# Kernel tuning notes

Hardware: AMD Instinct MI355X
Metric: run time of the kernel (lower is better)

Reference implementation:

```python
import jax, jax.numpy as jnp
import numpy as np

SPATIAL_SCALE = 0.25
N, C, H, W = 8, 256, 128, 128
P = 100000
IMG = 512.0  # image-space extent (H / spatial_scale)


def setup_inputs() -> dict:
    key = jax.random.key(0)
    k1, k2, k3, k4 = jax.random.split(key, 4)
    features = jax.random.normal(k1, (N, C, H, W), dtype=jnp.float32)
    batch_idx = jax.random.randint(k2, (P,), 0, N).astype(jnp.float32)
    xy = jax.random.uniform(k3, (P, 2), dtype=jnp.float32) * IMG
    rois = jnp.concatenate([batch_idx[:, None], xy], axis=1)  # [P,3]: (b, x, y)
    return {"features": features, "rois": rois}


def _interp(features, rois, spatial_scale):
    n, c, h, w = features.shape
    b = rois[:, 0].astype(jnp.int32)
    x = rois[:, 1] * spatial_scale
    y = rois[:, 2] * spatial_scale
    # RoIAlign-style bilinear interpolation with boundary handling
    valid = (y >= -1.0) & (y <= h) & (x >= -1.0) & (x <= w)
    y = jnp.maximum(y, 0.0)
    x = jnp.maximum(x, 0.0)
    y_low = jnp.floor(y).astype(jnp.int32)
    x_low = jnp.floor(x).astype(jnp.int32)
    y_at_edge = y_low >= h - 1
    x_at_edge = x_low >= w - 1
    y_low = jnp.minimum(y_low, h - 1)
    x_low = jnp.minimum(x_low, w - 1)
    y_high = jnp.where(y_at_edge, y_low, y_low + 1)
    x_high = jnp.where(x_at_edge, x_low, x_low + 1)
    y = jnp.where(y_at_edge, y_low.astype(y.dtype), y)
    x = jnp.where(x_at_edge, x_low.astype(x.dtype), x)
    ly = y - y_low
    lx = x - x_low
    hy = 1.0 - ly
    hx = 1.0 - lx
    w1 = (hy * hx)[:, None]  # [P,1]
    w2 = (hy * lx)[:, None]
    w3 = (ly * hx)[:, None]
    w4 = (ly * lx)[:, None]
    # fancy-index gather: [P, C] per corner
    v1 = features[b, :, y_low, x_low]
    v2 = features[b, :, y_low, x_high]
    v3 = features[b, :, y_high, x_low]
    v4 = features[b, :, y_high, x_high]
    out = w1 * v1 + w2 * v2 + w3 * v3 + w4 * v4  # [P, C]
    return jnp.where(valid[:, None], out, 0.0)


def reference(features, rois):
    return _interp(features, rois, SPATIAL_SCALE)
```

## Files before the change

kernel.cpp:

```cpp
#include <hip/hip_runtime.h>

#define SCALE   0.25f
#define NBATCH  8
#define CCH     256
#define HH      128
#define WW      128
#define NBUCK   (NBATCH * HH)
#define CAP     160

#define CG      64
#define NCG     (CCH / CG)


__global__ __launch_bounds__(1024) void k_bin(
    const float* __restrict__ rois, int* __restrict__ cnt,
    int4* __restrict__ slots, int P)
{
    __shared__ int lhist[NBUCK];
    __shared__ int lbase[NBUCK];
    const int t = threadIdx.x;
    lhist[t] = 0;
    __syncthreads();

    int p = blockIdx.x * 1024 + t;
    int mybk = -1, mypos = 0;
    int4 myrec = make_int4(0, 0, 0, 0);
    if (p < P) {
        float fb = rois[3 * p];
        float fx = rois[3 * p + 1] * SCALE;
        float fy = rois[3 * p + 2] * SCALE;
        int b = (int)fb;
        bool valid = (fy >= -1.0f) && (fy <= (float)HH) &&
                     (fx >= -1.0f) && (fx <= (float)WW);
        float y = fmaxf(fy, 0.0f);
        float x = fmaxf(fx, 0.0f);
        int ylo = (int)floorf(y);
        int xlo = (int)floorf(x);
        float yf = y, xf = x;
        int xhi;
        if (ylo >= HH - 1) { ylo = HH - 1; yf = (float)ylo; }
        if (xlo >= WW - 1) { xlo = WW - 1; xhi = WW - 1; xf = (float)xlo; }
        else               { xhi = xlo + 1; }
        float ly = yf - (float)ylo;
        float lx = xf - (float)xlo;
        unsigned pk = (unsigned)xlo | ((unsigned)xhi << 8) | (valid ? 0u : 0x80000000u);
        int bk = b * HH + ylo;
        mybk  = bk;
        mypos = atomicAdd(&lhist[bk], 1);
        myrec = make_int4(p, (int)pk, __float_as_int(lx), __float_as_int(ly));
    }
    __syncthreads();
    int h = lhist[t];
    lbase[t] = h ? atomicAdd(&cnt[t], h) : 0;
    __syncthreads();
    if (mybk >= 0) {
        int idx = lbase[mybk] + mypos;
        if (idx < CAP) slots[mybk * CAP + idx] = myrec;
    }
}

__global__ __launch_bounds__(1024, 8) void k_main(
    const float* __restrict__ feat, const int4* __restrict__ slots,
    const int* __restrict__ cnt_arr, float* __restrict__ out)
{
    const int bk = blockIdx.x & (NBUCK - 1);
    const int cg = blockIdx.x >> 10;
    const int cnt = min(cnt_arr[bk], CAP);
    if (cnt == 0) return;
    const int b  = bk >> 7;
    const int yl = bk & 127;
    const int yh = min(yl + 1, HH - 1);

    __shared__ __align__(16) float lds[2 * 128 * 64];
    float4* lds4 = (float4*)lds;

    const int t = threadIdx.x;

    {
        const int xq  = t & 31;
        const int cq  = (t >> 5) & 15;
        const int row = t >> 9;
        const int y   = row ? yh : yl;
        const float* g = feat + ((size_t)(b * CCH + cg * CG + 4 * cq) * HH + y) * WW + 4 * xq;
        float4 f0 = *(const float4*)(g);
        float4 f1 = *(const float4*)(g + HH * WW);
        float4 f2 = *(const float4*)(g + 2 * HH * WW);
        float4 f3 = *(const float4*)(g + 3 * HH * WW);
        const int slot = (cq + xq) & 15;
        float4* d = &lds4[(size_t)row * 2048 + (4 * xq) * 16 + slot];
        d[0]  = make_float4(f0.x, f1.x, f2.x, f3.x);
        d[16] = make_float4(f0.y, f1.y, f2.y, f3.y);
        d[32] = make_float4(f0.z, f1.z, f2.z, f3.z);
        d[48] = make_float4(f0.w, f1.w, f2.w, f3.w);
    }

    const int wv   = t >> 6;
    const int lane = t & 63;
    const int sub  = lane >> 4;
    const int cq   = lane & 15;
    const int4* sb = slots + bk * CAP;

    int  ii = wv * 4;
    int4 rc = make_int4(0, 0, 0, 0);
    if (ii < cnt) rc = sb[min(ii + sub, cnt - 1)];
    __syncthreads();

    for (; ii < cnt; ii += 64) {
        int4 r = rc;
        int jn = ii + 64;
        if (jn < cnt) rc = sb[min(jn + sub, cnt - 1)];

        bool act = (ii + sub < cnt);
        unsigned pk = (unsigned)r.y;
        float lx = __int_as_float(r.z);
        float ly = __int_as_float(r.w);
        float s  = ((int)pk < 0) ? 0.0f : 1.0f;
        float hy  = (1.0f - ly) * s;
        float lys = ly * s;
        float hx  = 1.0f - lx;
        float w1 = hy * hx, w2 = hy * lx, w3 = lys * hx, w4 = lys * lx;
        int xlo = pk & 255;
        int xhi = (pk >> 8) & 255;
        int alo = xlo * 16 + ((cq + (xlo >> 2)) & 15);
        int ahi = xhi * 16 + ((cq + (xhi >> 2)) & 15);

        float4 v1 = lds4[alo],        v2 = lds4[ahi];
        float4 v3 = lds4[2048 + alo], v4 = lds4[2048 + ahi];
        float4 o;
        o.x = w1 * v1.x + w2 * v2.x + w3 * v3.x + w4 * v4.x;
        o.y = w1 * v1.y + w2 * v2.y + w3 * v3.y + w4 * v4.y;
        o.z = w1 * v1.z + w2 * v2.z + w3 * v3.z + w4 * v4.z;
        o.w = w1 * v1.w + w2 * v2.w + w3 * v3.w + w4 * v4.w;

        if (act)
            *(float4*)(out + (size_t)r.x * CCH + cg * CG + 4 * cq) = o;
    }
}

extern "C" void kernel_launch(void* const* d_in, const int* in_sizes, int n_in,
                              void* d_out, int out_size, void* d_ws, size_t ws_size,
                              hipStream_t stream) {
    const float* feat = (const float*)d_in[0];
    const float* rois = (const float*)d_in[1];
    float* out = (float*)d_out;
    const int P = in_sizes[1] / 3;

    int*  cnt   = (int*)d_ws;
    int4* slots = (int4*)((char*)d_ws + NBUCK * sizeof(int));

    hipMemsetAsync(cnt, 0, NBUCK * sizeof(int), stream);
    const int bb = (P + 1023) / 1024;
    k_bin<<<bb, 1024, 0, stream>>>(rois, cnt, slots, P);
    k_main<<<NCG * NBUCK, 1024, 0, stream>>>(feat, slots, cnt, out);
}
```

Measured before the change: 235.1 us.

## Process 16 consecutive row buckets per block with a ring-buffered feature-row pipeline

Each block now handles a run of 16 y-buckets for one batch and channel group instead of a single bucket. It keeps a 4-slot shared-memory ring of feature rows, so adjacent buckets reuse the shared row and global loads of upcoming rows overlap with interpolation of the current one. This removes the duplicate load of each row (previously loaded as both y_high and y_low) and cuts block launch overhead. The cost is fewer blocks (256 versus 4096), which lowers parallelism and risks load imbalance, plus a barrier per row.

```diff
diff --git a/kernel.cpp b/kernel.cpp
--- a/kernel.cpp
+++ b/kernel.cpp
@@ -5,11 +5,14 @@
 #define CCH     256
 #define HH      128
 #define WW      128
+#define HW      (HH * WW)
 #define NBUCK   (NBATCH * HH)
 #define CAP     160
 
 #define CG      64
 #define NCG     (CCH / CG)
+#define BPB     16
+#define NSLOT   4
 
 
 __global__ __launch_bounds__(1024) void k_bin(
@@ -59,58 +62,54 @@
     }
 }
 
-__global__ __launch_bounds__(1024, 8) void k_main(
+struct R4 { float4 a, b, c, d; };
+
+__global__ __launch_bounds__(1024, 4) void k_main(
     const float* __restrict__ feat, const int4* __restrict__ slots,
     const int* __restrict__ cnt_arr, float* __restrict__ out)
 {
-    const int bk = blockIdx.x & (NBUCK - 1);
-    const int cg = blockIdx.x >> 10;
-    const int cnt = min(cnt_arr[bk], CAP);
-    if (cnt == 0) return;
-    const int b  = bk >> 7;
-    const int yl = bk & 127;
-    const int yh = min(yl + 1, HH - 1);
-
-    __shared__ __align__(16) float lds[2 * 128 * 64];
-    float4* lds4 = (float4*)lds;
-
-    const int t = threadIdx.x;
-
-    {
-        const int xq  = t & 31;
-        const int cq  = (t >> 5) & 15;
-        const int row = t >> 9;
-        const int y   = row ? yh : yl;
-        const float* g = feat + ((size_t)(b * CCH + cg * CG + 4 * cq) * HH + y) * WW + 4 * xq;
-        float4 f0 = *(const float4*)(g);
-        float4 f1 = *(const float4*)(g + HH * WW);
-        float4 f2 = *(const float4*)(g + 2 * HH * WW);
-        float4 f3 = *(const float4*)(g + 3 * HH * WW);
-        const int slot = (cq + xq) & 15;
-        float4* d = &lds4[(size_t)row * 2048 + (4 * xq) * 16 + slot];
-        d[0]  = make_float4(f0.x, f1.x, f2.x, f3.x);
-        d[16] = make_float4(f0.y, f1.y, f2.y, f3.y);
-        d[32] = make_float4(f0.z, f1.z, f2.z, f3.z);
-        d[48] = make_float4(f0.w, f1.w, f2.w, f3.w);
-    }
-
+    const int grp = blockIdx.x & (NBATCH * (HH / BPB) - 1);
+    const int cg  = blockIdx.x >> 6;
+    const int b   = grp >> 3;
+    const int y0  = (grp & 7) * BPB;
+    const int bk0 = b * HH + y0;
+
+    __shared__ __align__(16) float4 ring[NSLOT][WW][16];
+    __shared__ int scnt[BPB];
+
+    const int t    = threadIdx.x;
     const int wv   = t >> 6;
     const int lane = t & 63;
-    const int sub  = lane >> 4;
-    const int cq   = lane & 15;
-    const int4* sb = slots + bk * CAP;
-
-    int  ii = wv * 4;
-    int4 rc = make_int4(0, 0, 0, 0);
-    if (ii < cnt) rc = sb[min(ii + sub, cnt - 1)];
-    __syncthreads();
-
-    for (; ii < cnt; ii += 64) {
-        int4 r = rc;
-        int jn = ii + 64;
-        if (jn < cnt) rc = sb[min(jn + sub, cnt - 1)];
-
-        bool act = (ii + sub < cnt);
+    const bool stager = (t < 512);
+    const int sxq = t & 31;
+    const int scq = (t >> 5) & 15;
+
+    if (t < BPB) scnt[t] = min(cnt_arr[bk0 + t], CAP);
+
+    const float* gbase = feat + (size_t)(b * CCH + cg * CG + 4 * scq) * HW + 4 * sxq;
+
+#define LOAD_ROW(rr, reg) do { \
+        int y_ = min(y0 + (rr), HH - 1); \
+        const float* g_ = gbase + y_ * WW; \
+        (reg).a = *(const float4*)(g_); \
+        (reg).b = *(const float4*)(g_ + HW); \
+        (reg).c = *(const float4*)(g_ + 2 * HW); \
+        (reg).d = *(const float4*)(g_ + 3 * HW); \
+    } while (0)
+
+#define WRITE_ROW(slot, reg) do { \
+        float4* d_ = &ring[slot][4 * sxq][(scq + sxq) & 15]; \
+        d_[0]  = make_float4((reg).a.x, (reg).b.x, (reg).c.x, (reg).d.x); \
+        d_[16] = make_float4((reg).a.y, (reg).b.y, (reg).c.y, (reg).d.y); \
+        d_[32] = make_float4((reg).a.z, (reg).b.z, (reg).c.z, (reg).d.z); \
+        d_[48] = make_float4((reg).a.w, (reg).b.w, (reg).c.w, (reg).d.w); \
+    } while (0)
+
+    const int sub = lane >> 4;
+    const int cq  = lane & 15;
+    float* const outbase = out + cg * CG + 4 * cq;
+
+    auto process = [&](int4 r, const float4* lo, const float4* hi, bool act) {
         unsigned pk = (unsigned)r.y;
         float lx = __int_as_float(r.z);
         float ly = __int_as_float(r.w);
@@ -123,18 +122,66 @@
         int xhi = (pk >> 8) & 255;
         int alo = xlo * 16 + ((cq + (xlo >> 2)) & 15);
         int ahi = xhi * 16 + ((cq + (xhi >> 2)) & 15);
-
-        float4 v1 = lds4[alo],        v2 = lds4[ahi];
-        float4 v3 = lds4[2048 + alo], v4 = lds4[2048 + ahi];
+        float4 v1 = lo[alo], v2 = lo[ahi];
+        float4 v3 = hi[alo], v4 = hi[ahi];
         float4 o;
         o.x = w1 * v1.x + w2 * v2.x + w3 * v3.x + w4 * v4.x;
         o.y = w1 * v1.y + w2 * v2.y + w3 * v3.y + w4 * v4.y;
         o.z = w1 * v1.z + w2 * v2.z + w3 * v3.z + w4 * v4.z;
         o.w = w1 * v1.w + w2 * v2.w + w3 * v3.w + w4 * v4.w;
-
         if (act)
-            *(float4*)(out + (size_t)r.x * CCH + cg * CG + 4 * cq) = o;
-    }
+            *(float4*)(outbase + (size_t)r.x * CCH) = o;
+    };
+
+    R4 ra, rb;
+    if (stager) { LOAD_ROW(0, ra); LOAD_ROW(1, rb); }
+    const int4* sb = slots + (size_t)bk0 * CAP;
+    const int ii0 = wv * 4;
+    const int cnt0 = min(cnt_arr[bk0], CAP);
+    int4 rc0 = make_int4(0, (int)0x80000000u, 0, 0), rc1 = rc0;
+    if (cnt0 > 0) {
+        rc0 = sb[min(ii0 + sub, cnt0 - 1)];
+        rc1 = sb[min(ii0 + 64 + sub, cnt0 - 1)];
+    }
+    if (stager) { WRITE_ROW(0, ra); WRITE_ROW(1, rb); LOAD_ROW(2, ra); }
+    __syncthreads();
+
+    for (int i = 0; i < BPB; ++i) {
+        const int cnt_i = (i == 0) ? cnt0 : scnt[i];
+        const float4* lo = &ring[i & 3][0][0];
+        const float4* hi = &ring[(i + 1) & 3][0][0];
+        const int4* sbi = sb + i * CAP;
+
+        if (cnt_i > 0) {
+            if (ii0 < cnt_i)      process(rc0, lo, hi, ii0 + sub < cnt_i);
+            if (ii0 + 64 < cnt_i) process(rc1, lo, hi, ii0 + 64 + sub < cnt_i);
+            for (int ii = ii0 + 128; ii < cnt_i; ii += 64)
+                process(sbi[min(ii + sub, cnt_i - 1)], lo, hi, ii + sub < cnt_i);
+        }
+        if (i + 1 < BPB) {
+            const int cn = scnt[i + 1];
+            if (cn > 0) {
+                const int4* sbn = sbi + CAP;
+                rc0 = sbn[min(ii0 + sub, cn - 1)];
+                rc1 = sbn[min(ii0 + 64 + sub, cn - 1)];
+            }
+        }
+        if (stager) {
+            if (i + 2 <= BPB) {
+                if (i & 1) WRITE_ROW((i + 2) & 3, rb);
+                else       WRITE_ROW((i + 2) & 3, ra);
+            }
+            if (i + 3 <= BPB) {
+                if (i & 1) LOAD_ROW(i + 3, ra);
+                else       LOAD_ROW(i + 3, rb);
+            }
+        }
+        asm volatile("s_waitcnt lgkmcnt(0)" ::: "memory");
+        __builtin_amdgcn_s_barrier();
+        __builtin_amdgcn_sched_barrier(0);
+    }
+#undef LOAD_ROW
+#undef WRITE_ROW
 }
 
 extern "C" void kernel_launch(void* const* d_in, const int* in_sizes, int n_in,
@@ -151,5 +198,5 @@
     hipMemsetAsync(cnt, 0, NBUCK * sizeof(int), stream);
     const int bb = (P + 1023) / 1024;
     k_bin<<<bb, 1024, 0, stream>>>(rois, cnt, slots, P);
-    k_main<<<NCG * NBUCK, 1024, 0, stream>>>(feat, slots, cnt, out);
+    k_main<<<NCG * NBATCH * (HH / BPB), 1024, 0, stream>>>(feat, slots, cnt, out);
 }
```

New measurement: 244.1 us. 3.8% more time.

## Halve channel group per block, prefetch slot records early, use nontemporal output stores

Applied to the files above, without the earlier changes.

Each block now handles 32 channels with 512 threads instead of 64 channels with 1024 threads. That doubles the number of blocks and halves LDS use per block, which should raise occupancy and let more blocks overlap their feature loads. The first two slot records per lane are loaded before the feature tile is staged, hiding their latency behind the global loads. Output writes use nontemporal stores to avoid polluting cache. In exchange, the 8 KB of rois slot records per bucket are read twice as many times, since each bucket is now processed by twice as many channel groups.

```diff
diff --git a/kernel.cpp b/kernel.cpp
--- a/kernel.cpp
+++ b/kernel.cpp
@@ -5,11 +5,14 @@
 #define CCH     256
 #define HH      128
 #define WW      128
+#define HW      (HH * WW)
 #define NBUCK   (NBATCH * HH)
 #define CAP     160
 
-#define CG      64
+#define CG      32
 #define NCG     (CCH / CG)
+
+typedef float f32x4 __attribute__((ext_vector_type(4)));
 
 
 __global__ __launch_bounds__(1024) void k_bin(
@@ -59,58 +62,54 @@
     }
 }
 
-__global__ __launch_bounds__(1024, 8) void k_main(
+__global__ __launch_bounds__(512, 8) void k_main(
     const float* __restrict__ feat, const int4* __restrict__ slots,
     const int* __restrict__ cnt_arr, float* __restrict__ out)
 {
-    const int bk = blockIdx.x & (NBUCK - 1);
-    const int cg = blockIdx.x >> 10;
+    const int bk  = blockIdx.x & (NBUCK - 1);
+    const int cgp = blockIdx.x >> 10;
     const int cnt = min(cnt_arr[bk], CAP);
     if (cnt == 0) return;
     const int b  = bk >> 7;
     const int yl = bk & 127;
     const int yh = min(yl + 1, HH - 1);
 
-    __shared__ __align__(16) float lds[2 * 128 * 64];
-    float4* lds4 = (float4*)lds;
+    __shared__ __align__(16) float4 lds4[2][WW][8];
 
-    const int t = threadIdx.x;
+    const int t    = threadIdx.x;
+    const int wv   = t >> 6;
+    const int lane = t & 63;
+    const int sub  = lane >> 3;
+    const int cq   = lane & 7;
+
+    const int4* sb = slots + (size_t)bk * CAP;
+    const int ii0 = wv * 8;
+    int4 rc0 = sb[min(ii0 + sub, cnt - 1)];
+    int4 rc1 = sb[min(ii0 + 64 + sub, cnt - 1)];
 
     {
         const int xq  = t & 31;
-        const int cq  = (t >> 5) & 15;
-        const int row = t >> 9;
+        const int cq8 = (t >> 5) & 7;
+        const int row = t >> 8;
         const int y   = row ? yh : yl;
-        const float* g = feat + ((size_t)(b * CCH + cg * CG + 4 * cq) * HH + y) * WW + 4 * xq;
+        const float* g = feat + ((size_t)(b * CCH + cgp * CG + 4 * cq8) * HH + y) * WW + 4 * xq;
         float4 f0 = *(const float4*)(g);
-        float4 f1 = *(const float4*)(g + HH * WW);
-        float4 f2 = *(const float4*)(g + 2 * HH * WW);
-        float4 f3 = *(const float4*)(g + 3 * HH * WW);
-        const int slot = (cq + xq) & 15;
-        float4* d = &lds4[(size_t)row * 2048 + (4 * xq) * 16 + slot];
+        float4 f1 = *(const float4*)(g + HW);
+        float4 f2 = *(const float4*)(g + 2 * HW);
+        float4 f3 = *(const float4*)(g + 3 * HW);
+        float4* d = &lds4[row][4 * xq][(cq8 + xq) & 7];
         d[0]  = make_float4(f0.x, f1.x, f2.x, f3.x);
-        d[16] = make_float4(f0.y, f1.y, f2.y, f3.y);
-        d[32] = make_float4(f0.z, f1.z, f2.z, f3.z);
-        d[48] = make_float4(f0.w, f1.w, f2.w, f3.w);
+        d[8]  = make_float4(f0.y, f1.y, f2.y, f3.y);
+        d[16] = make_float4(f0.z, f1.z, f2.z, f3.z);
+        d[24] = make_float4(f0.w, f1.w, f2.w, f3.w);
     }
-
-    const int wv   = t >> 6;
-    const int lane = t & 63;
-    const int sub  = lane >> 4;
-    const int cq   = lane & 15;
-    const int4* sb = slots + bk * CAP;
-
-    int  ii = wv * 4;
-    int4 rc = make_int4(0, 0, 0, 0);
-    if (ii < cnt) rc = sb[min(ii + sub, cnt - 1)];
     __syncthreads();
 
-    for (; ii < cnt; ii += 64) {
-        int4 r = rc;
-        int jn = ii + 64;
-        if (jn < cnt) rc = sb[min(jn + sub, cnt - 1)];
+    const float4* lo = &lds4[0][0][0];
+    const float4* hi = &lds4[1][0][0];
+    float* const outbase = out + cgp * CG + 4 * cq;
 
-        bool act = (ii + sub < cnt);
+    auto process = [&](int4 r, bool act) {
         unsigned pk = (unsigned)r.y;
         float lx = __int_as_float(r.z);
         float ly = __int_as_float(r.w);
@@ -121,20 +120,24 @@
         float w1 = hy * hx, w2 = hy * lx, w3 = lys * hx, w4 = lys * lx;
         int xlo = pk & 255;
         int xhi = (pk >> 8) & 255;
-        int alo = xlo * 16 + ((cq + (xlo >> 2)) & 15);
-        int ahi = xhi * 16 + ((cq + (xhi >> 2)) & 15);
-
-        float4 v1 = lds4[alo],        v2 = lds4[ahi];
-        float4 v3 = lds4[2048 + alo], v4 = lds4[2048 + ahi];
-        float4 o;
+        int alo = xlo * 8 + ((cq + (xlo >> 2)) & 7);
+        int ahi = xhi * 8 + ((cq + (xhi >> 2)) & 7);
+        float4 v1 = lo[alo], v2 = lo[ahi];
+        float4 v3 = hi[alo], v4 = hi[ahi];
+        f32x4 o;
         o.x = w1 * v1.x + w2 * v2.x + w3 * v3.x + w4 * v4.x;
         o.y = w1 * v1.y + w2 * v2.y + w3 * v3.y + w4 * v4.y;
         o.z = w1 * v1.z + w2 * v2.z + w3 * v3.z + w4 * v4.z;
         o.w = w1 * v1.w + w2 * v2.w + w3 * v3.w + w4 * v4.w;
+        if (act)
+            __builtin_nontemporal_store(o, (f32x4*)(outbase + (size_t)r.x * CCH));
+    };
 
-        if (act)
-            *(float4*)(out + (size_t)r.x * CCH + cg * CG + 4 * cq) = o;
-    }
+    process(rc0, ii0 + sub < cnt);
+    if (ii0 + 64 < cnt)
+        process(rc1, ii0 + 64 + sub < cnt);
+    for (int ii = ii0 + 128; ii < cnt; ii += 64)
+        process(sb[min(ii + sub, cnt - 1)], ii + sub < cnt);
 }
 
 extern "C" void kernel_launch(void* const* d_in, const int* in_sizes, int n_in,
@@ -151,5 +154,5 @@
     hipMemsetAsync(cnt, 0, NBUCK * sizeof(int), stream);
     const int bb = (P + 1023) / 1024;
     k_bin<<<bb, 1024, 0, stream>>>(rois, cnt, slots, P);
-    k_main<<<NCG * NBUCK, 1024, 0, stream>>>(feat, slots, cnt, out);
+    k_main<<<NCG * NBUCK, 512, 0, stream>>>(feat, slots, cnt, out);
 }
```

Result: no change. 230.5 us (-1.9%).
